# Optimization experiments

Measured on AMD Instinct MI355X. Metric: run time of the kernel, lower is better.

Reference implementation:

```python
import jax, jax.numpy as jnp
import numpy as np

N_FEATURE = 1024
N_HEAD = 16
DK = N_FEATURE // N_HEAD
SCALE = float(np.sqrt(DK))
LN_EPS = 1e-5


def setup_inputs() -> dict:
    key = jax.random.key(0)
    ks = jax.random.split(key, 12)
    B, T, F = 4, 2048, N_FEATURE
    s = 1.0 / np.sqrt(F)
    inp = {
        "key": jax.random.normal(ks[0], (B, T, F), jnp.float32),
        "value": jax.random.normal(ks[1], (B, T, F), jnp.float32),
        "query": jax.random.normal(ks[2], (B, T, F), jnp.float32),
        "Wq": jax.random.uniform(ks[3], (F, F), jnp.float32, -s, s),
        "bq": jax.random.uniform(ks[4], (F,), jnp.float32, -s, s),
        "Wk": jax.random.uniform(ks[5], (F, F), jnp.float32, -s, s),
        "bk": jax.random.uniform(ks[6], (F,), jnp.float32, -s, s),
        "Wv": jax.random.uniform(ks[7], (F, F), jnp.float32, -s, s),
        "bv": jax.random.uniform(ks[8], (F,), jnp.float32, -s, s),
        "Wo": jax.random.uniform(ks[9], (F, F), jnp.float32, -s, s),
        "bo": jax.random.uniform(ks[10], (F,), jnp.float32, -s, s),
        "ln_g": jnp.ones((F,), jnp.float32),
        "ln_b": jnp.zeros((F,), jnp.float32),
    }
    return inp


def reference(key, value, query, Wq, bq, Wk, bk, Wv, bv, Wo, bo, ln_g, ln_b):
    # key/value/query: [B, T, F]. torch chunk(n_head, -1) == reshape to (B,T,H,dk).
    B, T, F = query.shape
    residual = query
    q = (query @ Wq.T + bq).reshape(B, T, N_HEAD, DK)
    k = (key @ Wk.T + bk).reshape(B, T, N_HEAD, DK)
    v = (value @ Wv.T + bv).reshape(B, T, N_HEAD, DK)
    # scores: [B, H, Tq, Tk]
    scores = jnp.einsum("bqhd,bkhd->bhqk", q, k) / SCALE
    attn = jax.nn.softmax(scores, axis=-1)
    ctx = jnp.einsum("bhqk,bkhd->bqhd", attn, v).reshape(B, T, F)
    out = ctx @ Wo.T + bo  # dropout in eval mode = identity
    x = residual + out
    mu = jnp.mean(x, axis=-1, keepdims=True)
    var = jnp.mean(jnp.square(x - mu), axis=-1, keepdims=True)
    return (x - mu) * jax.lax.rsqrt(var + LN_EPS) * ln_g + ln_b
```

## Files before the change

### kernel.cpp

```cpp
#include <hip/hip_runtime.h>
#include <hip/hip_bf16.h>
#include <cstdint>
#include <cstddef>

#define DEVI __device__ __forceinline__

typedef __attribute__((ext_vector_type(8))) short short8;
typedef __attribute__((ext_vector_type(4))) float f32x4;
typedef __attribute__((ext_vector_type(16))) float f32x16;
typedef __attribute__((ext_vector_type(4))) unsigned int u32x4;

constexpr int Bz = 4, Tt = 2048, Fd = 1024, Hh = 16, Dk = 64;
constexpr int Mrows = Bz * Tt;
constexpr float QSCALE = 0.18033688011112042f;

DEVI unsigned short f2bf(float f) {
  union { __hip_bfloat16 h; unsigned short u; } cv;
  cv.h = __float2bfloat16(f);
  return cv.u;
}

DEVI unsigned cvtpk(float a, float b) {
  unsigned r;
  asm("v_cvt_pk_bf16_f32 %0, %1, %2" : "=v"(r) : "v"(a), "v"(b));
  return r;
}

DEVI void gl_lds16(const void* g, void* s) {
  __builtin_amdgcn_global_load_lds(
      (const __attribute__((address_space(1))) void*)g,
      (__attribute__((address_space(3))) void*)s, 16, 0, 0);
}

__global__ void cvt4_bf16(const float* __restrict__ s0, unsigned short* __restrict__ d0,
                          const float* __restrict__ s1, unsigned short* __restrict__ d1,
                          const float* __restrict__ s2, unsigned short* __restrict__ d2,
                          const float* __restrict__ s3, unsigned short* __restrict__ d3,
                          int n4) {
  const float* src = blockIdx.y == 0 ? s0 : (blockIdx.y == 1 ? s1 : (blockIdx.y == 2 ? s2 : s3));
  unsigned short* dst = blockIdx.y == 0 ? d0 : (blockIdx.y == 1 ? d1 : (blockIdx.y == 2 ? d2 : d3));
  int i = blockIdx.x * blockDim.x + threadIdx.x;
  int stride = gridDim.x * blockDim.x;
  for (; i < n4; i += stride) {
    float4 v = reinterpret_cast<const float4*>(src)[i];
    ushort4 o;
    o.x = f2bf(v.x); o.y = f2bf(v.y); o.z = f2bf(v.z); o.w = f2bf(v.w);
    reinterpret_cast<ushort4*>(dst)[i] = o;
  }
}

__global__ __launch_bounds__(256, 2) void gemm_qkvf(
    const float* __restrict__ q32, const float* __restrict__ k32,
    const float* __restrict__ v32, const unsigned short* __restrict__ wq,
    const unsigned short* __restrict__ wk, const unsigned short* __restrict__ wv,
    const float* __restrict__ bq, const float* __restrict__ bk, const float* __restrict__ bv,
    unsigned short* __restrict__ Qb, unsigned short* __restrict__ Kb,
    unsigned short* __restrict__ Vt) {
  constexpr int K = 1024, N = 1024;
  __shared__ __align__(16) unsigned short As[128 * 64];
  __shared__ __align__(16) unsigned short Bs[128 * 64];
  int z = blockIdx.z;
  const float* A32 = z == 0 ? q32 : (z == 1 ? k32 : v32);
  const unsigned short* W = z == 0 ? wq : (z == 1 ? wk : wv);
  const float* bias = z == 0 ? bq : (z == 1 ? bk : bv);
  void* out = z == 0 ? (void*)Qb : (z == 1 ? (void*)Kb : (void*)Vt);
  float scale = z == 0 ? QSCALE : 1.0f;
  int mode = z == 2 ? 2 : 0;

  int f = blockIdx.y * gridDim.x + blockIdx.x;
  f = (f & 7) * 64 + (f >> 3);
  const int m0 = (f >> 3) * 128, n0 = (f & 7) * 128;
  const int t = threadIdx.x, w = t >> 6, l = t & 63;
  const int wr = w >> 1, wc = w & 1;
  const int lr = l & 15, lg = l >> 4;
  f32x4 acc[4][4] = {};

  for (int k0 = 0; k0 < K; k0 += 64) {
    __syncthreads();
    float4 fA[4][2];
#pragma unroll
    for (int i = 0; i < 4; ++i) {
      int row = i * 32 + w * 8 + (l >> 3);
      const float* src = A32 + (size_t)(m0 + row) * K + k0 + (l & 7) * 8;
      fA[i][0] = ((const float4*)src)[0];
      fA[i][1] = ((const float4*)src)[1];
    }
#pragma unroll
    for (int i = 0; i < 4; ++i) {
      int base = i * 4096 + w * 1024;
      int d = base + l * 16;
      int row = d >> 7;
      int srcb = ((l & 7) ^ (row & 7)) << 4;
      gl_lds16((const char*)W + ((size_t)(n0 + row) * K + k0) * 2 + srcb, (char*)Bs + base);
    }
#pragma unroll
    for (int i = 0; i < 4; ++i) {
      int row = i * 32 + w * 8 + (l >> 3);
      u32x4 wv4;
      wv4[0] = cvtpk(fA[i][0].x, fA[i][0].y);
      wv4[1] = cvtpk(fA[i][0].z, fA[i][0].w);
      wv4[2] = cvtpk(fA[i][1].x, fA[i][1].y);
      wv4[3] = cvtpk(fA[i][1].z, fA[i][1].w);
      int slot = (l & 7) ^ (row & 7);
      *(u32x4*)((char*)As + row * 128 + slot * 16) = wv4;
    }
    __syncthreads();
#pragma unroll
    for (int kk = 0; kk < 2; ++kk) {
      short8 af[4], bf[4];
#pragma unroll
      for (int i = 0; i < 4; ++i) {
        int ra = wr * 64 + i * 16 + lr;
        int rb = wc * 64 + i * 16 + lr;
        af[i] = *(const short8*)((const char*)As + ra * 128 + (((kk * 4 + lg) ^ (ra & 7)) << 4));
        bf[i] = *(const short8*)((const char*)Bs + rb * 128 + (((kk * 4 + lg) ^ (rb & 7)) << 4));
      }
#pragma unroll
      for (int mi = 0; mi < 4; ++mi)
#pragma unroll
        for (int ni = 0; ni < 4; ++ni)
          acc[mi][ni] = __builtin_amdgcn_mfma_f32_16x16x32_bf16(af[mi], bf[ni], acc[mi][ni], 0, 0, 0);
    }
  }
#pragma unroll
  for (int mi = 0; mi < 4; ++mi)
#pragma unroll
    for (int ni = 0; ni < 4; ++ni) {
      int col = n0 + wc * 64 + ni * 16 + lr;
      float bv = bias[col];
      if (mode == 2) {
        int hh = col >> 6, dd = col & 63;
        int row = m0 + wr * 64 + mi * 16 + lg * 4;
        int bb = row >> 11, t0 = row & 2047;
        ushort4 o;
        o.x = f2bf(acc[mi][ni][0] + bv);
        o.y = f2bf(acc[mi][ni][1] + bv);
        o.z = f2bf(acc[mi][ni][2] + bv);
        o.w = f2bf(acc[mi][ni][3] + bv);
        *(ushort4*)((unsigned short*)out + (((size_t)(bb * Hh + hh) * Dk + dd) << 11) + t0) = o;
      } else {
#pragma unroll
        for (int r = 0; r < 4; ++r) {
          int row = m0 + wr * 64 + mi * 16 + lg * 4 + r;
          ((unsigned short*)out)[(size_t)row * N + col] = f2bf((acc[mi][ni][r] + bv) * scale);
        }
      }
    }
}

__global__ __launch_bounds__(256, 2) void gemm_out(
    const unsigned short* __restrict__ A, const unsigned short* __restrict__ W,
    const float* __restrict__ bias, const float* __restrict__ resid,
    float* __restrict__ out) {
  constexpr int K = 1024, N = 1024;
  __shared__ __align__(16) unsigned short As[128 * 64];
  __shared__ __align__(16) unsigned short Bs[128 * 64];
  int f = blockIdx.y * gridDim.x + blockIdx.x;
  f = (f & 7) * 64 + (f >> 3);
  const int m0 = (f >> 3) * 128, n0 = (f & 7) * 128;
  const int t = threadIdx.x, w = t >> 6, l = t & 63;
  const int wr = w >> 1, wc = w & 1;
  const int lr = l & 15, lg = l >> 4;
  f32x4 acc[4][4] = {};
  for (int k0 = 0; k0 < K; k0 += 64) {
    __syncthreads();
#pragma unroll
    for (int i = 0; i < 4; ++i) {
      int base = i * 4096 + w * 1024;
      int d = base + l * 16;
      int row = d >> 7;
      int srcb = ((l & 7) ^ (row & 7)) << 4;
      gl_lds16((const char*)A + ((size_t)(m0 + row) * K + k0) * 2 + srcb, (char*)As + base);
      gl_lds16((const char*)W + ((size_t)(n0 + row) * K + k0) * 2 + srcb, (char*)Bs + base);
    }
    __syncthreads();
#pragma unroll
    for (int kk = 0; kk < 2; ++kk) {
      short8 af[4], bf[4];
#pragma unroll
      for (int i = 0; i < 4; ++i) {
        int ra = wr * 64 + i * 16 + lr;
        int rb = wc * 64 + i * 16 + lr;
        af[i] = *(const short8*)((const char*)As + ra * 128 + (((kk * 4 + lg) ^ (ra & 7)) << 4));
        bf[i] = *(const short8*)((const char*)Bs + rb * 128 + (((kk * 4 + lg) ^ (rb & 7)) << 4));
      }
#pragma unroll
      for (int mi = 0; mi < 4; ++mi)
#pragma unroll
        for (int ni = 0; ni < 4; ++ni)
          acc[mi][ni] = __builtin_amdgcn_mfma_f32_16x16x32_bf16(af[mi], bf[ni], acc[mi][ni], 0, 0, 0);
    }
  }
#pragma unroll
  for (int mi = 0; mi < 4; ++mi)
#pragma unroll
    for (int ni = 0; ni < 4; ++ni) {
      int col = n0 + wc * 64 + ni * 16 + lr;
      float bv = bias[col];
#pragma unroll
      for (int r = 0; r < 4; ++r) {
        int row = m0 + wr * 64 + mi * 16 + lg * 4 + r;
        size_t idx = (size_t)row * N + col;
        out[idx] = acc[mi][ni][r] + bv + resid[idx];
      }
    }
}

__global__ __launch_bounds__(256, 3) void attn_kernel(
    const unsigned short* __restrict__ Qb, const unsigned short* __restrict__ Kb,
    const unsigned short* __restrict__ Vt, unsigned short* __restrict__ Ctx) {
  __shared__ __align__(16) unsigned short Ks0[64 * 64], Ks1[64 * 64], Ks2[64 * 64];
  __shared__ __align__(16) unsigned short Vs0[64 * 64], Vs1[64 * 64], Vs2[64 * 64];
  int bid = blockIdx.x;
  bid = (bid & 7) * 128 + (bid >> 3);
  const int q0 = (bid & 15) * 128;
  const int h = (bid >> 4) & 15;
  const int b = bid >> 8;
  const int t = threadIdx.x, w = t >> 6, l = t & 63;
  const int q31 = l & 31, hi = l >> 5;
  const int qbase = q0 + w * 32;

  short8 qf[4];
  {
    const unsigned short* qp = Qb + (size_t)(b * Tt + qbase + q31) * Fd + h * Dk;
#pragma unroll
    for (int c = 0; c < 4; ++c) qf[c] = *(const short8*)(qp + c * 16 + hi * 8);
  }

  int koff[8];
#pragma unroll
  for (int g = 0; g < 2; ++g)
#pragma unroll
    for (int c = 0; c < 4; ++c) {
      int row = g * 32 + q31;
      koff[g * 4 + c] = row * 128 + ((c * 32 + hi * 16) ^ ((row & 7) << 4));
    }

  const size_t kbase = (size_t)(b * Tt) * Fd + h * Dk;
  const size_t vbase = (size_t)((b * Hh + h) * Dk) * Tt;

  f32x16 O0{}, O1{};
  float lsA = 0.f, lsB = 0.f;

  auto stage = [&](unsigned short* Kd, unsigned short* Vd, int kt) {
#pragma unroll
    for (int i = 0; i < 2; ++i) {
      int base = w * 2048 + i * 1024;
      int d0 = base + l * 16;
      int row = d0 >> 7, inb = d0 & 127;
      int srcb = inb ^ ((row & 7) << 4);
      gl_lds16((const char*)Kb + (kbase + (size_t)(kt * 64 + row) * Fd) * 2 + srcb, (char*)Kd + base);
      gl_lds16((const char*)Vt + (vbase + (size_t)row * Tt + kt * 64) * 2 + srcb, (char*)Vd + base);
    }
  };

  auto tile = [&](const unsigned short* Kd, const unsigned short* Vd) {
    f32x16 S0{}, S1{};
    __builtin_amdgcn_s_setprio(1);
#pragma unroll
    for (int c = 0; c < 4; ++c) {
      short8 k0 = *(const short8*)((const char*)Kd + koff[c]);
      short8 k1 = *(const short8*)((const char*)Kd + koff[4 + c]);
      S0 = __builtin_amdgcn_mfma_f32_32x32x16_bf16(k0, qf[c], S0, 0, 0, 0);
      S1 = __builtin_amdgcn_mfma_f32_32x32x16_bf16(k1, qf[c], S1, 0, 0, 0);
    }
    __builtin_amdgcn_s_setprio(0);
    unsigned pk0[8], pk1[8];
#pragma unroll
    for (int j = 0; j < 8; ++j) {
      int r = j * 2;
      float a0 = __builtin_amdgcn_exp2f(S0[r]);
      float a1 = __builtin_amdgcn_exp2f(S0[r + 1]);
      float b0 = __builtin_amdgcn_exp2f(S1[r]);
      float b1 = __builtin_amdgcn_exp2f(S1[r + 1]);
      lsA += a0 + a1;
      lsB += b0 + b1;
      pk0[j] = cvtpk(a0, a1);
      pk1[j] = cvtpk(b0, b1);
    }
    short8 pf[4];
#pragma unroll
    for (int kc = 0; kc < 2; ++kc) {
      unsigned a0 = pk0[kc * 4 + 0], a2 = pk0[kc * 4 + 2];
      unsigned a1 = pk0[kc * 4 + 1], a3 = pk0[kc * 4 + 3];
      asm("v_permlane32_swap_b32 %0, %1" : "+v"(a0), "+v"(a2));
      asm("v_permlane32_swap_b32 %0, %1" : "+v"(a1), "+v"(a3));
      unsigned b0 = pk1[kc * 4 + 0], b2 = pk1[kc * 4 + 2];
      unsigned b1 = pk1[kc * 4 + 1], b3 = pk1[kc * 4 + 3];
      asm("v_permlane32_swap_b32 %0, %1" : "+v"(b0), "+v"(b2));
      asm("v_permlane32_swap_b32 %0, %1" : "+v"(b1), "+v"(b3));
      u32x4 fa, fb;
      fa[0] = a0; fa[1] = a1; fa[2] = a2; fa[3] = a3;
      fb[0] = b0; fb[1] = b1; fb[2] = b2; fb[3] = b3;
      pf[kc] = __builtin_bit_cast(short8, fa);
      pf[2 + kc] = __builtin_bit_cast(short8, fb);
    }
    __builtin_amdgcn_s_setprio(1);
#pragma unroll
    for (int db = 0; db < 2; ++db)
#pragma unroll
      for (int kvc = 0; kvc < 4; ++kvc) {
        short8 vf = *(const short8*)((const char*)Vd + koff[db * 4 + kvc]);
        if (db == 0)
          O0 = __builtin_amdgcn_mfma_f32_32x32x16_bf16(vf, pf[kvc], O0, 0, 0, 0);
        else
          O1 = __builtin_amdgcn_mfma_f32_32x32x16_bf16(vf, pf[kvc], O1, 0, 0, 0);
      }
    __builtin_amdgcn_s_setprio(0);
  };

  stage(Ks0, Vs0, 0);
  stage(Ks1, Vs1, 1);
  unsigned short *kC = Ks0, *vC = Vs0;
  unsigned short *kN = Ks1, *vN = Vs1;
  unsigned short *kW = Ks2, *vW = Vs2;
  for (int kt = 0; kt < 30; ++kt) {
    asm volatile("s_waitcnt vmcnt(4)" ::: "memory");
    __builtin_amdgcn_s_barrier();
    stage(kW, vW, kt + 2);
    tile(kC, vC);
    unsigned short *tk = kC, *tv = vC;
    kC = kN; vC = vN;
    kN = kW; vN = vW;
    kW = tk; vW = tv;
  }
  asm volatile("s_waitcnt vmcnt(4)" ::: "memory");
  __builtin_amdgcn_s_barrier();
  tile(kC, vC);
  asm volatile("s_waitcnt vmcnt(0)" ::: "memory");
  __builtin_amdgcn_s_barrier();
  tile(kN, vN);
  __builtin_amdgcn_s_barrier();

  float lsum = lsA + lsB;
  lsum += __shfl_xor(lsum, 32);
  float linv = 1.0f / lsum;
  unsigned short* Ow = (w < 2 ? Ks0 : Ks1) + (w & 1) * 2048;
#pragma unroll
  for (int db = 0; db < 2; ++db)
#pragma unroll
    for (int rp = 0; rp < 8; ++rp) {
      int r = rp * 2;
      float a = (db == 0 ? O0[r] : O1[r]) * linv;
      float b2 = (db == 0 ? O0[r + 1] : O1[r + 1]) * linv;
      unsigned wv = cvtpk(a, b2);
      int dd = db * 32 + (r & 3) + 8 * (r >> 2) + 4 * hi;
      int byteo = (q31 * 128 + (dd >> 1) * 4) ^ ((q31 & 7) << 4);
      *(unsigned*)((char*)Ow + byteo) = wv;
    }
#pragma unroll
  for (int i = 0; i < 4; ++i) {
    int qq = i * 8 + (l >> 3), slot = l & 7;
    int byteo = (qq * 128 + slot * 16) ^ ((qq & 7) << 4);
    short8 ov = *(const short8*)((const char*)Ow + byteo);
    *(short8*)(Ctx + (size_t)(b * Tt + qbase + qq) * Fd + h * Dk + slot * 8) = ov;
  }
}

__global__ __launch_bounds__(256) void ln_res(
    float* __restrict__ xo, const float* __restrict__ gamma, const float* __restrict__ beta) {
  int row = blockIdx.x, t = threadIdx.x;
  float4 xv = ((const float4*)(xo + (size_t)row * Fd))[t];
  float x0 = xv.x, x1 = xv.y, x2 = xv.z, x3 = xv.w;
  float s = x0 + x1 + x2 + x3;
  float ss = x0 * x0 + x1 * x1 + x2 * x2 + x3 * x3;
#pragma unroll
  for (int off = 32; off >= 1; off >>= 1) {
    s += __shfl_xor(s, off);
    ss += __shfl_xor(ss, off);
  }
  __shared__ float rs_[4], rss[4];
  int w = t >> 6, l = t & 63;
  if (l == 0) { rs_[w] = s; rss[w] = ss; }
  __syncthreads();
  s = rs_[0] + rs_[1] + rs_[2] + rs_[3];
  ss = rss[0] + rss[1] + rss[2] + rss[3];
  float mu = s * (1.0f / 1024.0f);
  float var = ss * (1.0f / 1024.0f) - mu * mu;
  float rstd = rsqrtf(var + 1e-5f);
  float4 gv = ((const float4*)gamma)[t];
  float4 bv = ((const float4*)beta)[t];
  float4 o;
  o.x = (x0 - mu) * rstd * gv.x + bv.x;
  o.y = (x1 - mu) * rstd * gv.y + bv.y;
  o.z = (x2 - mu) * rstd * gv.z + bv.z;
  o.w = (x3 - mu) * rstd * gv.w + bv.w;
  ((float4*)(xo + (size_t)row * Fd))[t] = o;
}

extern "C" void kernel_launch(void* const* d_in, const int* in_sizes, int n_in,
                              void* d_out, int out_size, void* d_ws, size_t ws_size,
                              hipStream_t stream) {
  (void)in_sizes; (void)n_in; (void)out_size; (void)ws_size;
  const float* key   = (const float*)d_in[0];
  const float* value = (const float*)d_in[1];
  const float* query = (const float*)d_in[2];
  const float* Wq = (const float*)d_in[3];
  const float* bq = (const float*)d_in[4];
  const float* Wk = (const float*)d_in[5];
  const float* bk = (const float*)d_in[6];
  const float* Wv = (const float*)d_in[7];
  const float* bv_ = (const float*)d_in[8];
  const float* Wo = (const float*)d_in[9];
  const float* bo = (const float*)d_in[10];
  const float* ln_g = (const float*)d_in[11];
  const float* ln_b = (const float*)d_in[12];
  float* out = (float*)d_out;

  char* ws = (char*)d_ws;
  size_t off = 0;
  auto alloc = [&](size_t bytes) {
    char* p = ws + off;
    off += (bytes + 255) & ~(size_t)255;
    return p;
  };
  const size_t MF = (size_t)Mrows * Fd;
  unsigned short* Qb  = (unsigned short*)alloc(MF * 2);
  unsigned short* Kbf = (unsigned short*)alloc(MF * 2);
  unsigned short* Vtb = (unsigned short*)alloc(MF * 2);
  unsigned short* Ctx = (unsigned short*)alloc(MF * 2);
  unsigned short* wqb = (unsigned short*)alloc((size_t)Fd * Fd * 2);
  unsigned short* wkb = (unsigned short*)alloc((size_t)Fd * Fd * 2);
  unsigned short* wvb = (unsigned short*)alloc((size_t)Fd * Fd * 2);
  unsigned short* wob = (unsigned short*)alloc((size_t)Fd * Fd * 2);

  cvt4_bf16<<<dim3(256, 4), 256, 0, stream>>>(Wq, wqb, Wk, wkb, Wv, wvb, Wo, wob, (Fd * Fd) / 4);

  gemm_qkvf<<<dim3(Fd / 128, Mrows / 128, 3), 256, 0, stream>>>(
      query, key, value, wqb, wkb, wvb, bq, bk, bv_, Qb, Kbf, Vtb);

  attn_kernel<<<Bz * Hh * (Tt / 128), 256, 0, stream>>>(Qb, Kbf, Vtb, Ctx);

  gemm_out<<<dim3(Fd / 128, Mrows / 128), 256, 0, stream>>>(Ctx, wob, bo, query, out);
  ln_res<<<Mrows, 256, 0, stream>>>(out, ln_g, ln_b);
}
```

Measured before the change: 190.5 us.

## Double-buffer LDS tiles in QKV and output projection GEMMs

After: 190.7 us. No clear change (+0.1%).

```diff
diff --git a/kernel.cpp b/kernel.cpp
--- a/kernel.cpp
+++ b/kernel.cpp
@@ -57,8 +57,8 @@
     unsigned short* __restrict__ Qb, unsigned short* __restrict__ Kb,
     unsigned short* __restrict__ Vt) {
   constexpr int K = 1024, N = 1024;
-  __shared__ __align__(16) unsigned short As[128 * 64];
-  __shared__ __align__(16) unsigned short Bs[128 * 64];
+  __shared__ __align__(16) unsigned short As[2][128 * 64];
+  __shared__ __align__(16) unsigned short Bs[2][128 * 64];
   int z = blockIdx.z;
   const float* A32 = z == 0 ? q32 : (z == 1 ? k32 : v32);
   const unsigned short* W = z == 0 ? wq : (z == 1 ? wk : wv);
@@ -75,9 +75,7 @@
   const int lr = l & 15, lg = l >> 4;
   f32x4 acc[4][4] = {};
 
-  for (int k0 = 0; k0 < K; k0 += 64) {
-    __syncthreads();
-    float4 fA[4][2];
+  auto loadA = [&](int k0, float4 (&fA)[4][2]) {
 #pragma unroll
     for (int i = 0; i < 4; ++i) {
       int row = i * 32 + w * 8 + (l >> 3);
@@ -85,14 +83,18 @@
       fA[i][0] = ((const float4*)src)[0];
       fA[i][1] = ((const float4*)src)[1];
     }
+  };
+  auto stageB = [&](unsigned short* Bd, int k0) {
 #pragma unroll
     for (int i = 0; i < 4; ++i) {
       int base = i * 4096 + w * 1024;
       int d = base + l * 16;
       int row = d >> 7;
       int srcb = ((l & 7) ^ (row & 7)) << 4;
-      gl_lds16((const char*)W + ((size_t)(n0 + row) * K + k0) * 2 + srcb, (char*)Bs + base);
-    }
+      gl_lds16((const char*)W + ((size_t)(n0 + row) * K + k0) * 2 + srcb, (char*)Bd + base);
+    }
+  };
+  auto writeA = [&](unsigned short* Ad, const float4 (&fA)[4][2]) {
 #pragma unroll
     for (int i = 0; i < 4; ++i) {
       int row = i * 32 + w * 8 + (l >> 3);
@@ -102,26 +104,50 @@
       wv4[2] = cvtpk(fA[i][1].x, fA[i][1].y);
       wv4[3] = cvtpk(fA[i][1].z, fA[i][1].w);
       int slot = (l & 7) ^ (row & 7);
-      *(u32x4*)((char*)As + row * 128 + slot * 16) = wv4;
-    }
+      *(u32x4*)((char*)Ad + row * 128 + slot * 16) = wv4;
+    }
+  };
+  auto compute_half = [&](const unsigned short* Ab, const unsigned short* Bb, int kk) {
+    short8 af[4], bf[4];
+#pragma unroll
+    for (int i = 0; i < 4; ++i) {
+      int ra = wr * 64 + i * 16 + lr;
+      int rb = wc * 64 + i * 16 + lr;
+      af[i] = *(const short8*)((const char*)Ab + ra * 128 + (((kk * 4 + lg) ^ (ra & 7)) << 4));
+      bf[i] = *(const short8*)((const char*)Bb + rb * 128 + (((kk * 4 + lg) ^ (rb & 7)) << 4));
+    }
+#pragma unroll
+    for (int mi = 0; mi < 4; ++mi)
+#pragma unroll
+      for (int ni = 0; ni < 4; ++ni)
+        acc[mi][ni] = __builtin_amdgcn_mfma_f32_16x16x32_bf16(af[mi], bf[ni], acc[mi][ni], 0, 0, 0);
+  };
+
+  {
+    float4 f0[4][2];
+    loadA(0, f0);
+    stageB(Bs[0], 0);
+    writeA(As[0], f0);
+  }
+  __syncthreads();
+
+#pragma unroll 2
+  for (int kt = 0; kt < 16; ++kt) {
+    const unsigned short* Ac = As[kt & 1];
+    const unsigned short* Bc = Bs[kt & 1];
+    float4 fN[4][2];
+    if (kt < 15) {
+      loadA((kt + 1) * 64, fN);
+      stageB(Bs[(kt & 1) ^ 1], (kt + 1) * 64);
+    }
+    __builtin_amdgcn_sched_barrier(0);
+    compute_half(Ac, Bc, 0);
+    __builtin_amdgcn_sched_barrier(0);
+    if (kt < 15) writeA(As[(kt & 1) ^ 1], fN);
+    compute_half(Ac, Bc, 1);
     __syncthreads();
-#pragma unroll
-    for (int kk = 0; kk < 2; ++kk) {
-      short8 af[4], bf[4];
-#pragma unroll
-      for (int i = 0; i < 4; ++i) {
-        int ra = wr * 64 + i * 16 + lr;
-        int rb = wc * 64 + i * 16 + lr;
-        af[i] = *(const short8*)((const char*)As + ra * 128 + (((kk * 4 + lg) ^ (ra & 7)) << 4));
-        bf[i] = *(const short8*)((const char*)Bs + rb * 128 + (((kk * 4 + lg) ^ (rb & 7)) << 4));
-      }
-#pragma unroll
-      for (int mi = 0; mi < 4; ++mi)
-#pragma unroll
-        for (int ni = 0; ni < 4; ++ni)
-          acc[mi][ni] = __builtin_amdgcn_mfma_f32_16x16x32_bf16(af[mi], bf[ni], acc[mi][ni], 0, 0, 0);
-    }
-  }
+  }
+
 #pragma unroll
   for (int mi = 0; mi < 4; ++mi)
 #pragma unroll
@@ -153,8 +179,8 @@
     const float* __restrict__ bias, const float* __restrict__ resid,
     float* __restrict__ out) {
   constexpr int K = 1024, N = 1024;
-  __shared__ __align__(16) unsigned short As[128 * 64];
-  __shared__ __align__(16) unsigned short Bs[128 * 64];
+  __shared__ __align__(16) unsigned short As[2][128 * 64];
+  __shared__ __align__(16) unsigned short Bs[2][128 * 64];
   int f = blockIdx.y * gridDim.x + blockIdx.x;
   f = (f & 7) * 64 + (f >> 3);
   const int m0 = (f >> 3) * 128, n0 = (f & 7) * 128;
@@ -162,35 +188,46 @@
   const int wr = w >> 1, wc = w & 1;
   const int lr = l & 15, lg = l >> 4;
   f32x4 acc[4][4] = {};
-  for (int k0 = 0; k0 < K; k0 += 64) {
-    __syncthreads();
+
+  auto stage2 = [&](unsigned short* Ad, unsigned short* Bd, int k0) {
 #pragma unroll
     for (int i = 0; i < 4; ++i) {
       int base = i * 4096 + w * 1024;
       int d = base + l * 16;
       int row = d >> 7;
       int srcb = ((l & 7) ^ (row & 7)) << 4;
-      gl_lds16((const char*)A + ((size_t)(m0 + row) * K + k0) * 2 + srcb, (char*)As + base);
-      gl_lds16((const char*)W + ((size_t)(n0 + row) * K + k0) * 2 + srcb, (char*)Bs + base);
-    }
+      gl_lds16((const char*)A + ((size_t)(m0 + row) * K + k0) * 2 + srcb, (char*)Ad + base);
+      gl_lds16((const char*)W + ((size_t)(n0 + row) * K + k0) * 2 + srcb, (char*)Bd + base);
+    }
+  };
+  auto compute_half = [&](const unsigned short* Ab, const unsigned short* Bb, int kk) {
+    short8 af[4], bf[4];
+#pragma unroll
+    for (int i = 0; i < 4; ++i) {
+      int ra = wr * 64 + i * 16 + lr;
+      int rb = wc * 64 + i * 16 + lr;
+      af[i] = *(const short8*)((const char*)Ab + ra * 128 + (((kk * 4 + lg) ^ (ra & 7)) << 4));
+      bf[i] = *(const short8*)((const char*)Bb + rb * 128 + (((kk * 4 + lg) ^ (rb & 7)) << 4));
+    }
+#pragma unroll
+    for (int mi = 0; mi < 4; ++mi)
+#pragma unroll
+      for (int ni = 0; ni < 4; ++ni)
+        acc[mi][ni] = __builtin_amdgcn_mfma_f32_16x16x32_bf16(af[mi], bf[ni], acc[mi][ni], 0, 0, 0);
+  };
+
+  stage2(As[0], Bs[0], 0);
+  __syncthreads();
+
+#pragma unroll 2
+  for (int kt = 0; kt < 16; ++kt) {
+    if (kt < 15) stage2(As[(kt & 1) ^ 1], Bs[(kt & 1) ^ 1], (kt + 1) * 64);
+    __builtin_amdgcn_sched_barrier(0);
+    compute_half(As[kt & 1], Bs[kt & 1], 0);
+    compute_half(As[kt & 1], Bs[kt & 1], 1);
     __syncthreads();
-#pragma unroll
-    for (int kk = 0; kk < 2; ++kk) {
-      short8 af[4], bf[4];
-#pragma unroll
-      for (int i = 0; i < 4; ++i) {
-        int ra = wr * 64 + i * 16 + lr;
-        int rb = wc * 64 + i * 16 + lr;
-        af[i] = *(const short8*)((const char*)As + ra * 128 + (((kk * 4 + lg) ^ (ra & 7)) << 4));
-        bf[i] = *(const short8*)((const char*)Bs + rb * 128 + (((kk * 4 + lg) ^ (rb & 7)) << 4));
-      }
-#pragma unroll
-      for (int mi = 0; mi < 4; ++mi)
-#pragma unroll
-        for (int ni = 0; ni < 4; ++ni)
-          acc[mi][ni] = __builtin_amdgcn_mfma_f32_16x16x32_bf16(af[mi], bf[ni], acc[mi][ni], 0, 0, 0);
-    }
-  }
+  }
+
 #pragma unroll
   for (int mi = 0; mi < 4; ++mi)
 #pragma unroll
```

## Process 64 query rows per wave in attention to reuse K/V tiles

Applied to the files above, without the earlier changes.

New measurement: 183.1 us. 1.04x faster.

```diff
diff --git a/kernel.cpp b/kernel.cpp
--- a/kernel.cpp
+++ b/kernel.cpp
@@ -206,25 +206,34 @@
     }
 }
 
-__global__ __launch_bounds__(256, 3) void attn_kernel(
+__global__ __launch_bounds__(256, 2) void attn_kernel(
     const unsigned short* __restrict__ Qb, const unsigned short* __restrict__ Kb,
     const unsigned short* __restrict__ Vt, unsigned short* __restrict__ Ctx) {
-  __shared__ __align__(16) unsigned short Ks0[64 * 64], Ks1[64 * 64], Ks2[64 * 64];
-  __shared__ __align__(16) unsigned short Vs0[64 * 64], Vs1[64 * 64], Vs2[64 * 64];
+  __shared__ __align__(16) unsigned short smem[6 * 4096];
+  unsigned short* Ks0 = smem;
+  unsigned short* Ks1 = smem + 4096;
+  unsigned short* Ks2 = smem + 2 * 4096;
+  unsigned short* Vs0 = smem + 3 * 4096;
+  unsigned short* Vs1 = smem + 4 * 4096;
+  unsigned short* Vs2 = smem + 5 * 4096;
   int bid = blockIdx.x;
-  bid = (bid & 7) * 128 + (bid >> 3);
-  const int q0 = (bid & 15) * 128;
-  const int h = (bid >> 4) & 15;
-  const int b = bid >> 8;
+  bid = (bid & 7) * 64 + (bid >> 3);
+  const int q0 = (bid & 7) * 256;
+  const int h = (bid >> 3) & 15;
+  const int b = bid >> 7;
   const int t = threadIdx.x, w = t >> 6, l = t & 63;
   const int q31 = l & 31, hi = l >> 5;
-  const int qbase = q0 + w * 32;
-
-  short8 qf[4];
+  const int qbase = q0 + w * 64;
+
+  short8 qfA[4], qfB[4];
   {
-    const unsigned short* qp = Qb + (size_t)(b * Tt + qbase + q31) * Fd + h * Dk;
-#pragma unroll
-    for (int c = 0; c < 4; ++c) qf[c] = *(const short8*)(qp + c * 16 + hi * 8);
+    const unsigned short* qpA = Qb + (size_t)(b * Tt + qbase + q31) * Fd + h * Dk;
+    const unsigned short* qpB = qpA + (size_t)32 * Fd;
+#pragma unroll
+    for (int c = 0; c < 4; ++c) {
+      qfA[c] = *(const short8*)(qpA + c * 16 + hi * 8);
+      qfB[c] = *(const short8*)(qpB + c * 16 + hi * 8);
+    }
   }
 
   int koff[8];
@@ -239,8 +248,8 @@
   const size_t kbase = (size_t)(b * Tt) * Fd + h * Dk;
   const size_t vbase = (size_t)((b * Hh + h) * Dk) * Tt;
 
-  f32x16 O0{}, O1{};
-  float lsA = 0.f, lsB = 0.f;
+  f32x16 OA0{}, OA1{}, OB0{}, OB1{};
+  float lsA0 = 0.f, lsB0 = 0.f, lsA1 = 0.f, lsB1 = 0.f;
 
   auto stage = [&](unsigned short* Kd, unsigned short* Vd, int kt) {
 #pragma unroll
@@ -254,17 +263,7 @@
     }
   };
 
-  auto tile = [&](const unsigned short* Kd, const unsigned short* Vd) {
-    f32x16 S0{}, S1{};
-    __builtin_amdgcn_s_setprio(1);
-#pragma unroll
-    for (int c = 0; c < 4; ++c) {
-      short8 k0 = *(const short8*)((const char*)Kd + koff[c]);
-      short8 k1 = *(const short8*)((const char*)Kd + koff[4 + c]);
-      S0 = __builtin_amdgcn_mfma_f32_32x32x16_bf16(k0, qf[c], S0, 0, 0, 0);
-      S1 = __builtin_amdgcn_mfma_f32_32x32x16_bf16(k1, qf[c], S1, 0, 0, 0);
-    }
-    __builtin_amdgcn_s_setprio(0);
+  auto softmax_pack = [&](const f32x16& S0, const f32x16& S1, float& lsA, float& lsB, short8* pf) {
     unsigned pk0[8], pk1[8];
 #pragma unroll
     for (int j = 0; j < 8; ++j) {
@@ -278,7 +277,6 @@
       pk0[j] = cvtpk(a0, a1);
       pk1[j] = cvtpk(b0, b1);
     }
-    short8 pf[4];
 #pragma unroll
     for (int kc = 0; kc < 2; ++kc) {
       unsigned a0 = pk0[kc * 4 + 0], a2 = pk0[kc * 4 + 2];
@@ -295,16 +293,37 @@
       pf[kc] = __builtin_bit_cast(short8, fa);
       pf[2 + kc] = __builtin_bit_cast(short8, fb);
     }
+  };
+
+  auto tile = [&](const unsigned short* Kd, const unsigned short* Vd) {
+    f32x16 S0a{}, S1a{}, S0b{}, S1b{};
+    __builtin_amdgcn_s_setprio(1);
+#pragma unroll
+    for (int c = 0; c < 4; ++c) {
+      short8 k0 = *(const short8*)((const char*)Kd + koff[c]);
+      short8 k1 = *(const short8*)((const char*)Kd + koff[4 + c]);
+      S0a = __builtin_amdgcn_mfma_f32_32x32x16_bf16(k0, qfA[c], S0a, 0, 0, 0);
+      S1a = __builtin_amdgcn_mfma_f32_32x32x16_bf16(k1, qfA[c], S1a, 0, 0, 0);
+      S0b = __builtin_amdgcn_mfma_f32_32x32x16_bf16(k0, qfB[c], S0b, 0, 0, 0);
+      S1b = __builtin_amdgcn_mfma_f32_32x32x16_bf16(k1, qfB[c], S1b, 0, 0, 0);
+    }
+    __builtin_amdgcn_s_setprio(0);
+    short8 pfA[4], pfB[4];
+    softmax_pack(S0a, S1a, lsA0, lsB0, pfA);
+    softmax_pack(S0b, S1b, lsA1, lsB1, pfB);
     __builtin_amdgcn_s_setprio(1);
 #pragma unroll
     for (int db = 0; db < 2; ++db)
 #pragma unroll
       for (int kvc = 0; kvc < 4; ++kvc) {
         short8 vf = *(const short8*)((const char*)Vd + koff[db * 4 + kvc]);
-        if (db == 0)
-          O0 = __builtin_amdgcn_mfma_f32_32x32x16_bf16(vf, pf[kvc], O0, 0, 0, 0);
-        else
-          O1 = __builtin_amdgcn_mfma_f32_32x32x16_bf16(vf, pf[kvc], O1, 0, 0, 0);
+        if (db == 0) {
+          OA0 = __builtin_amdgcn_mfma_f32_32x32x16_bf16(vf, pfA[kvc], OA0, 0, 0, 0);
+          OB0 = __builtin_amdgcn_mfma_f32_32x32x16_bf16(vf, pfB[kvc], OB0, 0, 0, 0);
+        } else {
+          OA1 = __builtin_amdgcn_mfma_f32_32x32x16_bf16(vf, pfA[kvc], OA1, 0, 0, 0);
+          OB1 = __builtin_amdgcn_mfma_f32_32x32x16_bf16(vf, pfB[kvc], OB1, 0, 0, 0);
+        }
       }
     __builtin_amdgcn_s_setprio(0);
   };
@@ -332,24 +351,38 @@
   tile(kN, vN);
   __builtin_amdgcn_s_barrier();
 
-  float lsum = lsA + lsB;
-  lsum += __shfl_xor(lsum, 32);
-  float linv = 1.0f / lsum;
-  unsigned short* Ow = (w < 2 ? Ks0 : Ks1) + (w & 1) * 2048;
-#pragma unroll
-  for (int db = 0; db < 2; ++db)
-#pragma unroll
-    for (int rp = 0; rp < 8; ++rp) {
-      int r = rp * 2;
-      float a = (db == 0 ? O0[r] : O1[r]) * linv;
-      float b2 = (db == 0 ? O0[r + 1] : O1[r + 1]) * linv;
-      unsigned wv = cvtpk(a, b2);
-      int dd = db * 32 + (r & 3) + 8 * (r >> 2) + 4 * hi;
-      int byteo = (q31 * 128 + (dd >> 1) * 4) ^ ((q31 & 7) << 4);
-      *(unsigned*)((char*)Ow + byteo) = wv;
-    }
-#pragma unroll
-  for (int i = 0; i < 4; ++i) {
+  float ls0 = lsA0 + lsB0;
+  ls0 += __shfl_xor(ls0, 32);
+  float linv0 = 1.0f / ls0;
+  float ls1 = lsA1 + lsB1;
+  ls1 += __shfl_xor(ls1, 32);
+  float linv1 = 1.0f / ls1;
+  unsigned short* Ow = smem + w * 4096;
+#pragma unroll
+  for (int g = 0; g < 2; ++g) {
+    float linv = g == 0 ? linv0 : linv1;
+    int rowq = g * 32 + q31;
+#pragma unroll
+    for (int db = 0; db < 2; ++db)
+#pragma unroll
+      for (int rp = 0; rp < 8; ++rp) {
+        int r = rp * 2;
+        float a, b2;
+        if (g == 0) {
+          a = (db == 0 ? OA0[r] : OA1[r]) * linv;
+          b2 = (db == 0 ? OA0[r + 1] : OA1[r + 1]) * linv;
+        } else {
+          a = (db == 0 ? OB0[r] : OB1[r]) * linv;
+          b2 = (db == 0 ? OB0[r + 1] : OB1[r + 1]) * linv;
+        }
+        unsigned wv = cvtpk(a, b2);
+        int dd = db * 32 + (r & 3) + 8 * (r >> 2) + 4 * hi;
+        int byteo = (rowq * 128 + (dd >> 1) * 4) ^ ((rowq & 7) << 4);
+        *(unsigned*)((char*)Ow + byteo) = wv;
+      }
+  }
+#pragma unroll
+  for (int i = 0; i < 8; ++i) {
     int qq = i * 8 + (l >> 3), slot = l & 7;
     int byteo = (qq * 128 + slot * 16) ^ ((qq & 7) << 4);
     short8 ov = *(const short8*)((const char*)Ow + byteo);
@@ -429,7 +462,7 @@
   gemm_qkvf<<<dim3(Fd / 128, Mrows / 128, 3), 256, 0, stream>>>(
       query, key, value, wqb, wkb, wvb, bq, bk, bv_, Qb, Kbf, Vtb);
 
-  attn_kernel<<<Bz * Hh * (Tt / 128), 256, 0, stream>>>(Qb, Kbf, Vtb, Ctx);
+  attn_kernel<<<Bz * Hh * (Tt / 256), 256, 0, stream>>>(Qb, Kbf, Vtb, Ctx);
 
   gemm_out<<<dim3(Fd / 128, Mrows / 128), 256, 0, stream>>>(Ctx, wob, bo, query, out);
   ln_res<<<Mrows, 256, 0, stream>>>(out, ln_g, ln_b);
```

## Software-pipeline attention QK/PV and enlarge QKV GEMM and attention blocks

Applied to the files above, without the earlier changes.

After: 180.9 us. 5.0% less time.

```diff
diff --git a/kernel.cpp b/kernel.cpp
--- a/kernel.cpp
+++ b/kernel.cpp
@@ -49,7 +49,7 @@
   }
 }
 
-__global__ __launch_bounds__(256, 2) void gemm_qkvf(
+__global__ __launch_bounds__(512, 2) void gemm_qkvf(
     const float* __restrict__ q32, const float* __restrict__ k32,
     const float* __restrict__ v32, const unsigned short* __restrict__ wq,
     const unsigned short* __restrict__ wk, const unsigned short* __restrict__ wv,
@@ -58,7 +58,7 @@
     unsigned short* __restrict__ Vt) {
   constexpr int K = 1024, N = 1024;
   __shared__ __align__(16) unsigned short As[128 * 64];
-  __shared__ __align__(16) unsigned short Bs[128 * 64];
+  __shared__ __align__(16) unsigned short Bs[256 * 64];
   int z = blockIdx.z;
   const float* A32 = z == 0 ? q32 : (z == 1 ? k32 : v32);
   const unsigned short* W = z == 0 ? wq : (z == 1 ? wk : wv);
@@ -68,34 +68,34 @@
   int mode = z == 2 ? 2 : 0;
 
   int f = blockIdx.y * gridDim.x + blockIdx.x;
-  f = (f & 7) * 64 + (f >> 3);
-  const int m0 = (f >> 3) * 128, n0 = (f & 7) * 128;
+  f = (f & 7) * 32 + (f >> 3);
+  const int m0 = (f >> 2) * 128, n0 = (f & 3) * 256;
   const int t = threadIdx.x, w = t >> 6, l = t & 63;
-  const int wr = w >> 1, wc = w & 1;
+  const int wr = w >> 2, wc = w & 3;
   const int lr = l & 15, lg = l >> 4;
   f32x4 acc[4][4] = {};
 
   for (int k0 = 0; k0 < K; k0 += 64) {
     __syncthreads();
-    float4 fA[4][2];
-#pragma unroll
-    for (int i = 0; i < 4; ++i) {
-      int row = i * 32 + w * 8 + (l >> 3);
+    float4 fA[2][2];
+#pragma unroll
+    for (int i = 0; i < 2; ++i) {
+      int row = i * 64 + w * 8 + (l >> 3);
       const float* src = A32 + (size_t)(m0 + row) * K + k0 + (l & 7) * 8;
       fA[i][0] = ((const float4*)src)[0];
       fA[i][1] = ((const float4*)src)[1];
     }
 #pragma unroll
     for (int i = 0; i < 4; ++i) {
-      int base = i * 4096 + w * 1024;
+      int base = i * 8192 + w * 1024;
       int d = base + l * 16;
       int row = d >> 7;
       int srcb = ((l & 7) ^ (row & 7)) << 4;
       gl_lds16((const char*)W + ((size_t)(n0 + row) * K + k0) * 2 + srcb, (char*)Bs + base);
     }
 #pragma unroll
-    for (int i = 0; i < 4; ++i) {
-      int row = i * 32 + w * 8 + (l >> 3);
+    for (int i = 0; i < 2; ++i) {
+      int row = i * 64 + w * 8 + (l >> 3);
       u32x4 wv4;
       wv4[0] = cvtpk(fA[i][0].x, fA[i][0].y);
       wv4[1] = cvtpk(fA[i][0].z, fA[i][0].w);
@@ -206,16 +206,16 @@
     }
 }
 
-__global__ __launch_bounds__(256, 3) void attn_kernel(
+__global__ __launch_bounds__(512, 4) void attn_kernel(
     const unsigned short* __restrict__ Qb, const unsigned short* __restrict__ Kb,
     const unsigned short* __restrict__ Vt, unsigned short* __restrict__ Ctx) {
-  __shared__ __align__(16) unsigned short Ks0[64 * 64], Ks1[64 * 64], Ks2[64 * 64];
-  __shared__ __align__(16) unsigned short Vs0[64 * 64], Vs1[64 * 64], Vs2[64 * 64];
+  __shared__ __align__(16) unsigned short smem[8 * 4096];
   int bid = blockIdx.x;
-  bid = (bid & 7) * 128 + (bid >> 3);
-  const int q0 = (bid & 15) * 128;
-  const int h = (bid >> 4) & 15;
-  const int b = bid >> 8;
+  const int xcd = bid & 7, idx = bid >> 3;
+  const int bh = xcd * 8 + (idx >> 3);
+  const int q0 = (idx & 7) * 256;
+  const int h = bh & 15;
+  const int b = bh >> 4;
   const int t = threadIdx.x, w = t >> 6, l = t & 63;
   const int q31 = l & 31, hi = l >> 5;
   const int qbase = q0 + w * 32;
@@ -240,31 +240,53 @@
   const size_t vbase = (size_t)((b * Hh + h) * Dk) * Tt;
 
   f32x16 O0{}, O1{};
+  short8 pf[4];
   float lsA = 0.f, lsB = 0.f;
 
-  auto stage = [&](unsigned short* Kd, unsigned short* Vd, int kt) {
-#pragma unroll
-    for (int i = 0; i < 2; ++i) {
-      int base = w * 2048 + i * 1024;
-      int d0 = base + l * 16;
-      int row = d0 >> 7, inb = d0 & 127;
-      int srcb = inb ^ ((row & 7) << 4);
-      gl_lds16((const char*)Kb + (kbase + (size_t)(kt * 64 + row) * Fd) * 2 + srcb, (char*)Kd + base);
-      gl_lds16((const char*)Vt + (vbase + (size_t)row * Tt + kt * 64) * 2 + srcb, (char*)Vd + base);
-    }
+  auto kbuf = [&](int kt) { return (const char*)smem + ((kt & 3) << 13); };
+  auto vbuf = [&](int kt) { return (const char*)smem + 32768 + ((kt & 3) << 13); };
+
+  auto stage = [&](int kt) {
+    char* Kd = (char*)smem + ((kt & 3) << 13);
+    char* Vd = (char*)smem + 32768 + ((kt & 3) << 13);
+    int base = w * 1024;
+    int d0 = base + l * 16;
+    int row = d0 >> 7, inb = d0 & 127;
+    int srcb = inb ^ ((row & 7) << 4);
+    gl_lds16((const char*)Kb + (kbase + (size_t)(kt * 64 + row) * Fd) * 2 + srcb, Kd + base);
+    gl_lds16((const char*)Vt + (vbase + (size_t)row * Tt + kt * 64) * 2 + srcb, Vd + base);
   };
 
-  auto tile = [&](const unsigned short* Kd, const unsigned short* Vd) {
-    f32x16 S0{}, S1{};
+  auto qk = [&](int kt, f32x16& S0, f32x16& S1) {
+    const char* Kd = kbuf(kt);
     __builtin_amdgcn_s_setprio(1);
 #pragma unroll
     for (int c = 0; c < 4; ++c) {
-      short8 k0 = *(const short8*)((const char*)Kd + koff[c]);
-      short8 k1 = *(const short8*)((const char*)Kd + koff[4 + c]);
+      short8 k0 = *(const short8*)(Kd + koff[c]);
+      short8 k1 = *(const short8*)(Kd + koff[4 + c]);
       S0 = __builtin_amdgcn_mfma_f32_32x32x16_bf16(k0, qf[c], S0, 0, 0, 0);
       S1 = __builtin_amdgcn_mfma_f32_32x32x16_bf16(k1, qf[c], S1, 0, 0, 0);
     }
     __builtin_amdgcn_s_setprio(0);
+  };
+
+  auto pv = [&](int kt) {
+    const char* Vd = vbuf(kt);
+    __builtin_amdgcn_s_setprio(1);
+#pragma unroll
+    for (int db = 0; db < 2; ++db)
+#pragma unroll
+      for (int kvc = 0; kvc < 4; ++kvc) {
+        short8 vf = *(const short8*)(Vd + koff[db * 4 + kvc]);
+        if (db == 0)
+          O0 = __builtin_amdgcn_mfma_f32_32x32x16_bf16(vf, pf[kvc], O0, 0, 0, 0);
+        else
+          O1 = __builtin_amdgcn_mfma_f32_32x32x16_bf16(vf, pf[kvc], O1, 0, 0, 0);
+      }
+    __builtin_amdgcn_s_setprio(0);
+  };
+
+  auto softmax_pack = [&](const f32x16& S0, const f32x16& S1) {
     unsigned pk0[8], pk1[8];
 #pragma unroll
     for (int j = 0; j < 8; ++j) {
@@ -278,7 +300,6 @@
       pk0[j] = cvtpk(a0, a1);
       pk1[j] = cvtpk(b0, b1);
     }
-    short8 pf[4];
 #pragma unroll
     for (int kc = 0; kc < 2; ++kc) {
       unsigned a0 = pk0[kc * 4 + 0], a2 = pk0[kc * 4 + 2];
@@ -295,47 +316,42 @@
       pf[kc] = __builtin_bit_cast(short8, fa);
       pf[2 + kc] = __builtin_bit_cast(short8, fb);
     }
-    __builtin_amdgcn_s_setprio(1);
-#pragma unroll
-    for (int db = 0; db < 2; ++db)
-#pragma unroll
-      for (int kvc = 0; kvc < 4; ++kvc) {
-        short8 vf = *(const short8*)((const char*)Vd + koff[db * 4 + kvc]);
-        if (db == 0)
-          O0 = __builtin_amdgcn_mfma_f32_32x32x16_bf16(vf, pf[kvc], O0, 0, 0, 0);
-        else
-          O1 = __builtin_amdgcn_mfma_f32_32x32x16_bf16(vf, pf[kvc], O1, 0, 0, 0);
-      }
-    __builtin_amdgcn_s_setprio(0);
   };
 
-  stage(Ks0, Vs0, 0);
-  stage(Ks1, Vs1, 1);
-  unsigned short *kC = Ks0, *vC = Vs0;
-  unsigned short *kN = Ks1, *vN = Vs1;
-  unsigned short *kW = Ks2, *vW = Vs2;
-  for (int kt = 0; kt < 30; ++kt) {
-    asm volatile("s_waitcnt vmcnt(4)" ::: "memory");
+  stage(0);
+  stage(1);
+  asm volatile("s_waitcnt vmcnt(2)" ::: "memory");
+  __builtin_amdgcn_s_barrier();
+  stage(2);
+  {
+    f32x16 S0{}, S1{};
+    qk(0, S0, S1);
+    softmax_pack(S0, S1);
+  }
+  for (int kt = 1; kt < 31; ++kt) {
+    asm volatile("s_waitcnt vmcnt(2)" ::: "memory");
     __builtin_amdgcn_s_barrier();
-    stage(kW, vW, kt + 2);
-    tile(kC, vC);
-    unsigned short *tk = kC, *tv = vC;
-    kC = kN; vC = vN;
-    kN = kW; vN = vW;
-    kW = tk; vW = tv;
-  }
-  asm volatile("s_waitcnt vmcnt(4)" ::: "memory");
-  __builtin_amdgcn_s_barrier();
-  tile(kC, vC);
+    if (kt < 30) stage(kt + 2);
+    f32x16 S0{}, S1{};
+    qk(kt, S0, S1);
+    pv(kt - 1);
+    softmax_pack(S0, S1);
+  }
   asm volatile("s_waitcnt vmcnt(0)" ::: "memory");
   __builtin_amdgcn_s_barrier();
-  tile(kN, vN);
+  {
+    f32x16 S0{}, S1{};
+    qk(31, S0, S1);
+    pv(30);
+    softmax_pack(S0, S1);
+  }
+  pv(31);
   __builtin_amdgcn_s_barrier();
 
   float lsum = lsA + lsB;
   lsum += __shfl_xor(lsum, 32);
   float linv = 1.0f / lsum;
-  unsigned short* Ow = (w < 2 ? Ks0 : Ks1) + (w & 1) * 2048;
+  unsigned short* Ow = smem + w * 2048;
 #pragma unroll
   for (int db = 0; db < 2; ++db)
 #pragma unroll
@@ -426,10 +442,10 @@
 
   cvt4_bf16<<<dim3(256, 4), 256, 0, stream>>>(Wq, wqb, Wk, wkb, Wv, wvb, Wo, wob, (Fd * Fd) / 4);
 
-  gemm_qkvf<<<dim3(Fd / 128, Mrows / 128, 3), 256, 0, stream>>>(
+  gemm_qkvf<<<dim3(Fd / 256, Mrows / 128, 3), 512, 0, stream>>>(
       query, key, value, wqb, wkb, wvb, bq, bk, bv_, Qb, Kbf, Vtb);
 
-  attn_kernel<<<Bz * Hh * (Tt / 128), 256, 0, stream>>>(Qb, Kbf, Vtb, Ctx);
+  attn_kernel<<<Bz * Hh * (Tt / 256), 512, 0, stream>>>(Qb, Kbf, Vtb, Ctx);
 
   gemm_out<<<dim3(Fd / 128, Mrows / 128), 256, 0, stream>>>(Ctx, wob, bo, query, out);
   ln_res<<<Mrows, 256, 0, stream>>>(out, ln_g, ln_b);
```
